# Optimization experiments

Hardware: AMD Instinct MI355X
Metric: run time of the kernel (lower is better)

## Reference

```python
import jax, jax.numpy as jnp
import numpy as np

E = 8        # num_experts
TOP_K = 2    # num_experts_per_tok
H = 2048     # hidden_size
I = 1408     # moe_intermediate_size

def setup_inputs() -> dict:
    key = jax.random.key(0)
    k0, k1, k2, k3, k4 = jax.random.split(key, 5)
    hidden_states = jax.random.normal(k0, (2, 2048, H), dtype=jnp.float32)
    gate_w = jax.random.normal(k1, (E, H), dtype=jnp.float32) * 0.02   # router: Linear(H, E)
    wg = jax.random.normal(k2, (E, I, H), dtype=jnp.float32) * 0.02    # gate_proj per expert
    wu = jax.random.normal(k3, (E, I, H), dtype=jnp.float32) * 0.02    # up_proj per expert
    wd = jax.random.normal(k4, (E, H, I), dtype=jnp.float32) * 0.02    # down_proj per expert
    return {"hidden_states": hidden_states, "gate_w": gate_w, "wg": wg, "wu": wu, "wd": wd}

def reference(hidden_states, gate_w, wg, wu, wd):
    b, s, h = hidden_states.shape
    x = hidden_states.reshape(-1, h)                      # [T, H]
    router_logits = x @ gate_w.T                          # [T, E]
    routing_weights = jax.nn.softmax(router_logits.astype(jnp.float32), axis=-1)
    topk_weight, topk_idx = jax.lax.top_k(routing_weights, TOP_K)   # [T, K]
    topk_weight = topk_weight / jnp.sum(topk_weight, axis=-1, keepdims=True)
    # per-token combine weight for each expert: w[t,e] = sum_k topk_weight[t,k] * [topk_idx[t,k]==e]
    comb = jnp.sum(jax.nn.one_hot(topk_idx, E, dtype=x.dtype) * topk_weight[..., None].astype(x.dtype), axis=1)  # [T, E]
    # compute each expert on all tokens (dense faithful equivalent of masked dispatch), combine with comb
    def expert_out(e):
        g = x @ wg[e].T                                   # [T, I]
        u = x @ wu[e].T                                   # [T, I]
        return (jax.nn.silu(g) * u) @ wd[e].T             # [T, H]
    y = jnp.zeros_like(x)
    for e in range(E):  # small fixed expert count
        y = y + expert_out(e) * comb[:, e:e+1]
    final = y.reshape(b, s, h)
    return final, router_logits.astype(hidden_states.dtype)
```

## Files before the change

kernel.cpp:

```cpp
#include <hip/hip_runtime.h>

#define NTOK 4096
#define NEXP 8
#define HD 2048
#define ID 1408

typedef unsigned short u16;
typedef __attribute__((ext_vector_type(8))) short short8;
typedef __attribute__((ext_vector_type(4))) float f32x4;
typedef const __attribute__((address_space(1))) void* gas_ptr;
typedef __attribute__((address_space(3))) void* las_ptr;

__device__ __forceinline__ u16 f2bf(float f) {
  unsigned int u = __float_as_uint(f);
  u += 0x7FFFu + ((u >> 16) & 1u);
  return (u16)(u >> 16);
}

__device__ __forceinline__ void async16(const u16* g, u16* l) {
  __builtin_amdgcn_global_load_lds((gas_ptr)g, (las_ptr)l, 16, 0, 0);
}

__global__ void cvt_kernel(const float* __restrict__ s, u16* __restrict__ d, long n8) {
  long i = (long)blockIdx.x * blockDim.x + threadIdx.x;
  if (i >= n8) return;
  const float4* s4 = (const float4*)s;
  float4 a = s4[2*i], b = s4[2*i+1];
  short8 o;
  o[0] = (short)f2bf(a.x); o[1] = (short)f2bf(a.y);
  o[2] = (short)f2bf(a.z); o[3] = (short)f2bf(a.w);
  o[4] = (short)f2bf(b.x); o[5] = (short)f2bf(b.y);
  o[6] = (short)f2bf(b.z); o[7] = (short)f2bf(b.w);
  *(short8*)(d + 8*i) = o;
}

__global__ void router_kernel(const float* __restrict__ x, const float* __restrict__ gw,
                              float* __restrict__ logits, int* __restrict__ cnt,
                              int* __restrict__ ptok, float* __restrict__ pw) {
  int t = blockIdx.x * 4 + (threadIdx.x >> 6);
  int lane = threadIdx.x & 63;
  if (t >= NTOK) return;
  const float4* xr = (const float4*)(x + (size_t)t * HD);
  float dot[NEXP];
#pragma unroll
  for (int e = 0; e < NEXP; ++e) dot[e] = 0.f;
#pragma unroll
  for (int c = 0; c < 8; ++c) {
    float4 xv = xr[c*64 + lane];
#pragma unroll
    for (int e = 0; e < NEXP; ++e) {
      float4 gv = ((const float4*)(gw + e*HD))[c*64 + lane];
      dot[e] += xv.x*gv.x + xv.y*gv.y + xv.z*gv.z + xv.w*gv.w;
    }
  }
#pragma unroll
  for (int off = 32; off > 0; off >>= 1) {
#pragma unroll
    for (int e = 0; e < NEXP; ++e) dot[e] += __shfl_xor(dot[e], off);
  }
  if (lane < NEXP) logits[(size_t)t*NEXP + lane] = dot[lane];
  if (lane == 0) {
    float mx = dot[0];
#pragma unroll
    for (int e = 1; e < NEXP; ++e) mx = fmaxf(mx, dot[e]);
    float p[NEXP];
#pragma unroll
    for (int e = 0; e < NEXP; ++e) p[e] = __expf(dot[e] - mx);
    int e0 = 0;
#pragma unroll
    for (int e = 1; e < NEXP; ++e) if (p[e] > p[e0]) e0 = e;
    int e1 = (e0 == 0) ? 1 : 0;
#pragma unroll
    for (int e = 0; e < NEXP; ++e) if (e != e0 && p[e] > p[e1]) e1 = e;
    float denom = p[e0] + p[e1];
    int pos0 = atomicAdd(&cnt[e0], 1);
    ptok[e0*NTOK + pos0] = t; pw[e0*NTOK + pos0] = p[e0] / denom;
    int pos1 = atomicAdd(&cnt[e1], 1);
    ptok[e1*NTOK + pos1] = t; pw[e1*NTOK + pos1] = p[e1] / denom;
  }
}

__global__ void prefix_kernel(const int* __restrict__ cnt, int* __restrict__ offs) {
  if (threadIdx.x == 0) {
    int a = 0;
    for (int e = 0; e < NEXP; ++e) { offs[e] = a; a += cnt[e]; }
  }
}

__global__ __launch_bounds__(256, 2) void gemm1_kernel(
    const u16* __restrict__ xb, const u16* __restrict__ wgb, const u16* __restrict__ wub,
    const int* __restrict__ cnt, const int* __restrict__ offs,
    const int* __restrict__ ptok, u16* __restrict__ hbuf) {
  int e = blockIdx.z, mt = blockIdx.y, nt = blockIdx.x;
  int c = cnt[e];
  if (mt * 128 >= c) return;
  int off = offs[e];

  __shared__ u16 sA[128*32], sBg[128*32], sBu[128*32];

  int tid = threadIdx.x;
  int r0 = tid >> 2;
  int ch = (tid & 3) * 8;
  int s0 = mt*128 + r0, s1 = s0 + 64;
  int t0 = ptok[e*NTOK + (s0 < c ? s0 : 0)];
  int t1 = ptok[e*NTOK + (s1 < c ? s1 : 0)];
  const u16* ga0 = xb + (size_t)t0*HD + ch;
  const u16* ga1 = xb + (size_t)t1*HD + ch;
  int n0 = nt*128 + r0;
  const u16* gg0 = wgb + ((size_t)e*ID + n0)*HD + ch;
  const u16* gg1 = gg0 + (size_t)64*HD;
  const u16* gu0 = wub + ((size_t)e*ID + n0)*HD + ch;
  const u16* gu1 = gu0 + (size_t)64*HD;

  int lane = tid & 63, wv = tid >> 6, wr = wv >> 1, wc = wv & 1;
  int fm = lane & 15, kg = lane >> 4;

  f32x4 accg[4][4], accu[4][4];
#pragma unroll
  for (int i = 0; i < 4; ++i)
#pragma unroll
    for (int j = 0; j < 4; ++j) {
      accg[i][j] = {0.f, 0.f, 0.f, 0.f};
      accu[i][j] = {0.f, 0.f, 0.f, 0.f};
    }

  const u16* sAf  = sA  + (wr*64 + fm)*32 + kg*8;
  const u16* sBgf = sBg + (wc*64 + fm)*32 + kg*8;
  const u16* sBuf = sBu + (wc*64 + fm)*32 + kg*8;

  for (int k0 = 0; k0 < HD; k0 += 32) {
    async16(ga0 + k0, sA + tid*8);
    async16(ga1 + k0, sA + 2048 + tid*8);
    async16(gg0 + k0, sBg + tid*8);
    async16(gg1 + k0, sBg + 2048 + tid*8);
    async16(gu0 + k0, sBu + tid*8);
    async16(gu1 + k0, sBu + 2048 + tid*8);
    __syncthreads();
    short8 af[4], bg[4], bu[4];
#pragma unroll
    for (int i = 0; i < 4; ++i) af[i] = *(const short8*)(sAf + i*512);
#pragma unroll
    for (int j = 0; j < 4; ++j) {
      bg[j] = *(const short8*)(sBgf + j*512);
      bu[j] = *(const short8*)(sBuf + j*512);
    }
#pragma unroll
    for (int i = 0; i < 4; ++i)
#pragma unroll
      for (int j = 0; j < 4; ++j) {
        accg[i][j] = __builtin_amdgcn_mfma_f32_16x16x32_bf16(af[i], bg[j], accg[i][j], 0, 0, 0);
        accu[i][j] = __builtin_amdgcn_mfma_f32_16x16x32_bf16(af[i], bu[j], accu[i][j], 0, 0, 0);
      }
    __syncthreads();
  }

#pragma unroll
  for (int i = 0; i < 4; ++i) {
#pragma unroll
    for (int r = 0; r < 4; ++r) {
      int slot = mt*128 + wr*64 + i*16 + kg*4 + r;
      if (slot < c) {
        size_t rowb = (size_t)(off + slot) * ID + nt*128 + wc*64 + fm;
#pragma unroll
        for (int j = 0; j < 4; ++j) {
          float g = accg[i][j][r], u = accu[i][j][r];
          float hh = g * u / (1.f + __expf(-g));
          hbuf[rowb + (size_t)j*16] = f2bf(hh);
        }
      }
    }
  }
}

__global__ __launch_bounds__(256, 2) void gemm2_kernel(
    const u16* __restrict__ hbuf, const u16* __restrict__ wdb,
    const int* __restrict__ cnt, const int* __restrict__ offs,
    const int* __restrict__ ptok, const float* __restrict__ pw,
    float* __restrict__ out) {
  int e = blockIdx.z, mt = blockIdx.y, nt = blockIdx.x;
  int c = cnt[e];
  if (mt * 128 >= c) return;
  int off = offs[e];

  __shared__ u16 sA[128*32], sB[128*32];

  int tid = threadIdx.x;
  int r0 = tid >> 2;
  int ch = (tid & 3) * 8;
  int s0 = mt*128 + r0, s1 = s0 + 64;
  const u16* ga0 = hbuf + (size_t)(off + (s0 < c ? s0 : 0))*ID + ch;
  const u16* ga1 = hbuf + (size_t)(off + (s1 < c ? s1 : 0))*ID + ch;
  int n0 = nt*128 + r0;
  const u16* gb0 = wdb + ((size_t)e*HD + n0)*ID + ch;
  const u16* gb1 = gb0 + (size_t)64*ID;

  int lane = tid & 63, wv = tid >> 6, wr = wv >> 1, wc = wv & 1;
  int fm = lane & 15, kg = lane >> 4;

  f32x4 acc[4][4];
#pragma unroll
  for (int i = 0; i < 4; ++i)
#pragma unroll
    for (int j = 0; j < 4; ++j) acc[i][j] = {0.f, 0.f, 0.f, 0.f};

  const u16* sAf = sA + (wr*64 + fm)*32 + kg*8;
  const u16* sBf = sB + (wc*64 + fm)*32 + kg*8;

  for (int k0 = 0; k0 < ID; k0 += 32) {
    async16(ga0 + k0, sA + tid*8);
    async16(ga1 + k0, sA + 2048 + tid*8);
    async16(gb0 + k0, sB + tid*8);
    async16(gb1 + k0, sB + 2048 + tid*8);
    __syncthreads();
    short8 af[4], bf[4];
#pragma unroll
    for (int i = 0; i < 4; ++i) af[i] = *(const short8*)(sAf + i*512);
#pragma unroll
    for (int j = 0; j < 4; ++j) bf[j] = *(const short8*)(sBf + j*512);
#pragma unroll
    for (int i = 0; i < 4; ++i)
#pragma unroll
      for (int j = 0; j < 4; ++j)
        acc[i][j] = __builtin_amdgcn_mfma_f32_16x16x32_bf16(af[i], bf[j], acc[i][j], 0, 0, 0);
    __syncthreads();
  }

#pragma unroll
  for (int i = 0; i < 4; ++i) {
#pragma unroll
    for (int r = 0; r < 4; ++r) {
      int slot = mt*128 + wr*64 + i*16 + kg*4 + r;
      if (slot < c) {
        int tok = ptok[e*NTOK + slot];
        float wgt = pw[e*NTOK + slot];
        float* orow = out + (size_t)tok*HD + nt*128 + wc*64 + fm;
#pragma unroll
        for (int j = 0; j < 4; ++j)
          atomicAdd(orow + j*16, wgt * acc[i][j][r]);
      }
    }
  }
}

extern "C" void kernel_launch(void* const* d_in, const int* in_sizes, int n_in,
                              void* d_out, int out_size, void* d_ws, size_t ws_size,
                              hipStream_t stream) {
  const float* x  = (const float*)d_in[0];
  const float* gw = (const float*)d_in[1];
  const float* wg = (const float*)d_in[2];
  const float* wu = (const float*)d_in[3];
  const float* wd = (const float*)d_in[4];
  float* out = (float*)d_out;

  char* p = (char*)d_ws;
  u16*   xb   = (u16*)(p);
  u16*   wgb  = (u16*)(p + 16777216UL);
  u16*   wub  = (u16*)(p + 62914560UL);
  u16*   wdb  = (u16*)(p + 109051904UL);
  u16*   hbuf = (u16*)(p + 155189248UL);
  int*   ptok = (int*)(p + 178257920UL);
  float* pww  = (float*)(p + 178388992UL);
  int*   cnt  = (int*)(p + 178520064UL);
  int*   offs = (int*)(p + 178520320UL);

  hipMemsetAsync(out, 0, (size_t)NTOK * HD * sizeof(float), stream);
  hipMemsetAsync(cnt, 0, NEXP * sizeof(int), stream);

  cvt_kernel<<<4096, 256, 0, stream>>>(x, xb, (long)NTOK * HD / 8);
  cvt_kernel<<<11264, 256, 0, stream>>>(wg, wgb, (long)NEXP * ID * HD / 8);
  cvt_kernel<<<11264, 256, 0, stream>>>(wu, wub, (long)NEXP * ID * HD / 8);
  cvt_kernel<<<11264, 256, 0, stream>>>(wd, wdb, (long)NEXP * HD * ID / 8);

  router_kernel<<<1024, 256, 0, stream>>>(x, gw, out + (size_t)NTOK * HD, cnt, ptok, pww);
  prefix_kernel<<<1, 64, 0, stream>>>(cnt, offs);

  gemm1_kernel<<<dim3(11, 32, 8), 256, 0, stream>>>(xb, wgb, wub, cnt, offs, ptok, hbuf);
  gemm2_kernel<<<dim3(16, 32, 8), 256, 0, stream>>>(hbuf, wdb, cnt, offs, ptok, pww, out);
}
```

Before: 695.6 us.

## Widen GEMM K-tile to 64 with XOR-swizzled LDS, fuse conversions into router

Both expert GEMMs now stage 64-wide K slices instead of 32, which halves the number of barrier pairs per tile. The LDS layout uses an XOR swizzle on 16-byte chunks to avoid bank conflicts on fragment reads. The three weight conversions are merged into one launch, and the activation bf16 conversion is folded into the router kernel, which removes a separate pass over x. gemm2's launch bound is raised to 3 blocks per CU even though it uses more shared memory, which may pressure registers or limit occupancy.

```diff
diff --git a/kernel.cpp b/kernel.cpp
--- a/kernel.cpp
+++ b/kernel.cpp
@@ -7,6 +7,7 @@
 
 typedef unsigned short u16;
 typedef __attribute__((ext_vector_type(8))) short short8;
+typedef __attribute__((ext_vector_type(4))) short short4v;
 typedef __attribute__((ext_vector_type(4))) float f32x4;
 typedef const __attribute__((address_space(1))) void* gas_ptr;
 typedef __attribute__((address_space(3))) void* las_ptr;
@@ -21,32 +22,44 @@
   __builtin_amdgcn_global_load_lds((gas_ptr)g, (las_ptr)l, 16, 0, 0);
 }
 
-__global__ void cvt_kernel(const float* __restrict__ s, u16* __restrict__ d, long n8) {
+__global__ void cvt3_kernel(const float* __restrict__ s0, const float* __restrict__ s1,
+                            const float* __restrict__ s2, u16* __restrict__ d0,
+                            u16* __restrict__ d1, u16* __restrict__ d2, long n8each) {
   long i = (long)blockIdx.x * blockDim.x + threadIdx.x;
-  if (i >= n8) return;
+  const float* s; u16* d; long j;
+  if (i < n8each)            { s = s0; d = d0; j = i; }
+  else if (i < 2*n8each)     { s = s1; d = d1; j = i - n8each; }
+  else if (i < 3*n8each)     { s = s2; d = d2; j = i - 2*n8each; }
+  else return;
   const float4* s4 = (const float4*)s;
-  float4 a = s4[2*i], b = s4[2*i+1];
+  float4 a = s4[2*j], b = s4[2*j+1];
   short8 o;
   o[0] = (short)f2bf(a.x); o[1] = (short)f2bf(a.y);
   o[2] = (short)f2bf(a.z); o[3] = (short)f2bf(a.w);
   o[4] = (short)f2bf(b.x); o[5] = (short)f2bf(b.y);
   o[6] = (short)f2bf(b.z); o[7] = (short)f2bf(b.w);
-  *(short8*)(d + 8*i) = o;
+  *(short8*)(d + 8*j) = o;
 }
 
 __global__ void router_kernel(const float* __restrict__ x, const float* __restrict__ gw,
+                              u16* __restrict__ xb,
                               float* __restrict__ logits, int* __restrict__ cnt,
                               int* __restrict__ ptok, float* __restrict__ pw) {
   int t = blockIdx.x * 4 + (threadIdx.x >> 6);
   int lane = threadIdx.x & 63;
   if (t >= NTOK) return;
   const float4* xr = (const float4*)(x + (size_t)t * HD);
+  u16* xbr = xb + (size_t)t * HD;
   float dot[NEXP];
 #pragma unroll
   for (int e = 0; e < NEXP; ++e) dot[e] = 0.f;
 #pragma unroll
   for (int c = 0; c < 8; ++c) {
     float4 xv = xr[c*64 + lane];
+    short4v o;
+    o[0] = (short)f2bf(xv.x); o[1] = (short)f2bf(xv.y);
+    o[2] = (short)f2bf(xv.z); o[3] = (short)f2bf(xv.w);
+    *(short4v*)(xbr + (c*64 + lane)*4) = o;
 #pragma unroll
     for (int e = 0; e < NEXP; ++e) {
       float4 gv = ((const float4*)(gw + e*HD))[c*64 + lane];
@@ -96,24 +109,27 @@
   if (mt * 128 >= c) return;
   int off = offs[e];
 
-  __shared__ u16 sA[128*32], sBg[128*32], sBu[128*32];
+  __shared__ u16 sA[128*64], sBg[128*64], sBu[128*64];
 
   int tid = threadIdx.x;
-  int r0 = tid >> 2;
-  int ch = (tid & 3) * 8;
-  int s0 = mt*128 + r0, s1 = s0 + 64;
-  int t0 = ptok[e*NTOK + (s0 < c ? s0 : 0)];
-  int t1 = ptok[e*NTOK + (s1 < c ? s1 : 0)];
-  const u16* ga0 = xb + (size_t)t0*HD + ch;
-  const u16* ga1 = xb + (size_t)t1*HD + ch;
-  int n0 = nt*128 + r0;
-  const u16* gg0 = wgb + ((size_t)e*ID + n0)*HD + ch;
-  const u16* gg1 = gg0 + (size_t)64*HD;
-  const u16* gu0 = wub + ((size_t)e*ID + n0)*HD + ch;
-  const u16* gu1 = gu0 + (size_t)64*HD;
+  int r  = tid >> 3;
+  int cq = tid & 7;
+  int cx = (cq ^ (r & 7)) * 8;
+
+  const u16* ga[4];
+#pragma unroll
+  for (int p = 0; p < 4; ++p) {
+    int s = mt*128 + r + p*32;
+    int t = ptok[e*NTOK + (s < c ? s : 0)];
+    ga[p] = xb + (size_t)t*HD + cx;
+  }
+  int n0 = nt*128 + r;
+  const u16* gg = wgb + ((size_t)e*ID + n0)*HD + cx;
+  const u16* gu = wub + ((size_t)e*ID + n0)*HD + cx;
 
   int lane = tid & 63, wv = tid >> 6, wr = wv >> 1, wc = wv & 1;
   int fm = lane & 15, kg = lane >> 4;
+  int sw = fm & 7;
 
   f32x4 accg[4][4], accu[4][4];
 #pragma unroll
@@ -124,47 +140,48 @@
       accu[i][j] = {0.f, 0.f, 0.f, 0.f};
     }
 
-  const u16* sAf  = sA  + (wr*64 + fm)*32 + kg*8;
-  const u16* sBgf = sBg + (wc*64 + fm)*32 + kg*8;
-  const u16* sBuf = sBu + (wc*64 + fm)*32 + kg*8;
-
-  for (int k0 = 0; k0 < HD; k0 += 32) {
-    async16(ga0 + k0, sA + tid*8);
-    async16(ga1 + k0, sA + 2048 + tid*8);
-    async16(gg0 + k0, sBg + tid*8);
-    async16(gg1 + k0, sBg + 2048 + tid*8);
-    async16(gu0 + k0, sBu + tid*8);
-    async16(gu1 + k0, sBu + 2048 + tid*8);
+  for (int k0 = 0; k0 < HD; k0 += 64) {
+#pragma unroll
+    for (int p = 0; p < 4; ++p) {
+      async16(ga[p] + k0,                 sA  + p*2048 + tid*8);
+      async16(gg + (size_t)p*32*HD + k0,  sBg + p*2048 + tid*8);
+      async16(gu + (size_t)p*32*HD + k0,  sBu + p*2048 + tid*8);
+    }
     __syncthreads();
-    short8 af[4], bg[4], bu[4];
-#pragma unroll
-    for (int i = 0; i < 4; ++i) af[i] = *(const short8*)(sAf + i*512);
-#pragma unroll
-    for (int j = 0; j < 4; ++j) {
-      bg[j] = *(const short8*)(sBgf + j*512);
-      bu[j] = *(const short8*)(sBuf + j*512);
-    }
-#pragma unroll
-    for (int i = 0; i < 4; ++i)
+#pragma unroll
+    for (int h = 0; h < 2; ++h) {
+      int co = ((kg + 4*h) ^ sw) * 8;
+      short8 af[4], bg[4], bu[4];
+#pragma unroll
+      for (int i = 0; i < 4; ++i)
+        af[i] = *(const short8*)(sA + (wr*64 + i*16 + fm)*64 + co);
 #pragma unroll
       for (int j = 0; j < 4; ++j) {
-        accg[i][j] = __builtin_amdgcn_mfma_f32_16x16x32_bf16(af[i], bg[j], accg[i][j], 0, 0, 0);
-        accu[i][j] = __builtin_amdgcn_mfma_f32_16x16x32_bf16(af[i], bu[j], accu[i][j], 0, 0, 0);
+        bg[j] = *(const short8*)(sBg + (wc*64 + j*16 + fm)*64 + co);
+        bu[j] = *(const short8*)(sBu + (wc*64 + j*16 + fm)*64 + co);
       }
+#pragma unroll
+      for (int i = 0; i < 4; ++i)
+#pragma unroll
+        for (int j = 0; j < 4; ++j) {
+          accg[i][j] = __builtin_amdgcn_mfma_f32_16x16x32_bf16(af[i], bg[j], accg[i][j], 0, 0, 0);
+          accu[i][j] = __builtin_amdgcn_mfma_f32_16x16x32_bf16(af[i], bu[j], accu[i][j], 0, 0, 0);
+        }
+    }
     __syncthreads();
   }
 
 #pragma unroll
   for (int i = 0; i < 4; ++i) {
 #pragma unroll
-    for (int r = 0; r < 4; ++r) {
-      int slot = mt*128 + wr*64 + i*16 + kg*4 + r;
+    for (int rr = 0; rr < 4; ++rr) {
+      int slot = mt*128 + wr*64 + i*16 + kg*4 + rr;
       if (slot < c) {
         size_t rowb = (size_t)(off + slot) * ID + nt*128 + wc*64 + fm;
 #pragma unroll
         for (int j = 0; j < 4; ++j) {
-          float g = accg[i][j][r], u = accu[i][j][r];
-          float hh = g * u / (1.f + __expf(-g));
+          float gv = accg[i][j][rr], uv = accu[i][j][rr];
+          float hh = gv * uv / (1.f + __expf(-gv));
           hbuf[rowb + (size_t)j*16] = f2bf(hh);
         }
       }
@@ -172,7 +189,7 @@
   }
 }
 
-__global__ __launch_bounds__(256, 2) void gemm2_kernel(
+__global__ __launch_bounds__(256, 3) void gemm2_kernel(
     const u16* __restrict__ hbuf, const u16* __restrict__ wdb,
     const int* __restrict__ cnt, const int* __restrict__ offs,
     const int* __restrict__ ptok, const float* __restrict__ pw,
@@ -182,20 +199,25 @@
   if (mt * 128 >= c) return;
   int off = offs[e];
 
-  __shared__ u16 sA[128*32], sB[128*32];
+  __shared__ u16 sA[128*64], sB[128*64];
 
   int tid = threadIdx.x;
-  int r0 = tid >> 2;
-  int ch = (tid & 3) * 8;
-  int s0 = mt*128 + r0, s1 = s0 + 64;
-  const u16* ga0 = hbuf + (size_t)(off + (s0 < c ? s0 : 0))*ID + ch;
-  const u16* ga1 = hbuf + (size_t)(off + (s1 < c ? s1 : 0))*ID + ch;
-  int n0 = nt*128 + r0;
-  const u16* gb0 = wdb + ((size_t)e*HD + n0)*ID + ch;
-  const u16* gb1 = gb0 + (size_t)64*ID;
+  int r  = tid >> 3;
+  int cq = tid & 7;
+  int cx = (cq ^ (r & 7)) * 8;
+
+  const u16* ga[4];
+#pragma unroll
+  for (int p = 0; p < 4; ++p) {
+    int s = mt*128 + r + p*32;
+    ga[p] = hbuf + (size_t)(off + (s < c ? s : 0))*ID + cx;
+  }
+  int n0 = nt*128 + r;
+  const u16* gb = wdb + ((size_t)e*HD + n0)*ID + cx;
 
   int lane = tid & 63, wv = tid >> 6, wr = wv >> 1, wc = wv & 1;
   int fm = lane & 15, kg = lane >> 4;
+  int sw = fm & 7;
 
   f32x4 acc[4][4];
 #pragma unroll
@@ -203,40 +225,44 @@
 #pragma unroll
     for (int j = 0; j < 4; ++j) acc[i][j] = {0.f, 0.f, 0.f, 0.f};
 
-  const u16* sAf = sA + (wr*64 + fm)*32 + kg*8;
-  const u16* sBf = sB + (wc*64 + fm)*32 + kg*8;
-
-  for (int k0 = 0; k0 < ID; k0 += 32) {
-    async16(ga0 + k0, sA + tid*8);
-    async16(ga1 + k0, sA + 2048 + tid*8);
-    async16(gb0 + k0, sB + tid*8);
-    async16(gb1 + k0, sB + 2048 + tid*8);
+  for (int k0 = 0; k0 < ID; k0 += 64) {
+#pragma unroll
+    for (int p = 0; p < 4; ++p) {
+      async16(ga[p] + k0,                sA + p*2048 + tid*8);
+      async16(gb + (size_t)p*32*ID + k0, sB + p*2048 + tid*8);
+    }
     __syncthreads();
-    short8 af[4], bf[4];
-#pragma unroll
-    for (int i = 0; i < 4; ++i) af[i] = *(const short8*)(sAf + i*512);
-#pragma unroll
-    for (int j = 0; j < 4; ++j) bf[j] = *(const short8*)(sBf + j*512);
-#pragma unroll
-    for (int i = 0; i < 4; ++i)
+#pragma unroll
+    for (int h = 0; h < 2; ++h) {
+      int co = ((kg + 4*h) ^ sw) * 8;
+      short8 af[4], bf[4];
+#pragma unroll
+      for (int i = 0; i < 4; ++i)
+        af[i] = *(const short8*)(sA + (wr*64 + i*16 + fm)*64 + co);
 #pragma unroll
       for (int j = 0; j < 4; ++j)
-        acc[i][j] = __builtin_amdgcn_mfma_f32_16x16x32_bf16(af[i], bf[j], acc[i][j], 0, 0, 0);
+        bf[j] = *(const short8*)(sB + (wc*64 + j*16 + fm)*64 + co);
+#pragma unroll
+      for (int i = 0; i < 4; ++i)
+#pragma unroll
+        for (int j = 0; j < 4; ++j)
+          acc[i][j] = __builtin_amdgcn_mfma_f32_16x16x32_bf16(af[i], bf[j], acc[i][j], 0, 0, 0);
+    }
     __syncthreads();
   }
 
 #pragma unroll
   for (int i = 0; i < 4; ++i) {
 #pragma unroll
-    for (int r = 0; r < 4; ++r) {
-      int slot = mt*128 + wr*64 + i*16 + kg*4 + r;
+    for (int rr = 0; rr < 4; ++rr) {
+      int slot = mt*128 + wr*64 + i*16 + kg*4 + rr;
       if (slot < c) {
         int tok = ptok[e*NTOK + slot];
         float wgt = pw[e*NTOK + slot];
         float* orow = out + (size_t)tok*HD + nt*128 + wc*64 + fm;
 #pragma unroll
         for (int j = 0; j < 4; ++j)
-          atomicAdd(orow + j*16, wgt * acc[i][j][r]);
+          atomicAdd(orow + j*16, wgt * acc[i][j][rr]);
       }
     }
   }
@@ -266,12 +292,10 @@
   hipMemsetAsync(out, 0, (size_t)NTOK * HD * sizeof(float), stream);
   hipMemsetAsync(cnt, 0, NEXP * sizeof(int), stream);
 
-  cvt_kernel<<<4096, 256, 0, stream>>>(x, xb, (long)NTOK * HD / 8);
-  cvt_kernel<<<11264, 256, 0, stream>>>(wg, wgb, (long)NEXP * ID * HD / 8);
-  cvt_kernel<<<11264, 256, 0, stream>>>(wu, wub, (long)NEXP * ID * HD / 8);
-  cvt_kernel<<<11264, 256, 0, stream>>>(wd, wdb, (long)NEXP * HD * ID / 8);
-
-  router_kernel<<<1024, 256, 0, stream>>>(x, gw, out + (size_t)NTOK * HD, cnt, ptok, pww);
+  long n8each = (long)NEXP * ID * HD / 8;
+  cvt3_kernel<<<33792, 256, 0, stream>>>(wg, wu, wd, wgb, wub, wdb, n8each);
+
+  router_kernel<<<1024, 256, 0, stream>>>(x, gw, xb, out + (size_t)NTOK * HD, cnt, ptok, pww);
   prefix_kernel<<<1, 64, 0, stream>>>(cnt, offs);
 
   gemm1_kernel<<<dim3(11, 32, 8), 256, 0, stream>>>(xb, wgb, wub, cnt, offs, ptok, hbuf);
```

New measurement: 652.3 us. -6.2%, faster.
